# Kernel tuning notes

Hardware: AMD Instinct MI355X
Metric: run time of the kernel (lower is better)

## Reference

```python
import jax, jax.numpy as jnp
import numpy as np

B, H, W = 8, 56, 56
DIM_IN = 1792 + 2   # concatenated pyramid channels + 2 coord channels
D_OUT = 1792 // 4   # gamma_d = 4
N_CENTERS = H * W   # gamma_c = 1
K = 3


def avg_pool3(x):
    # F.avg_pool2d(x, 3, 1, 1) with count_include_pad=True: padded sum / 9
    s = jax.lax.reduce_window(x, 0.0, jax.lax.add, (1, 1, 3, 3), (1, 1, 1, 1),
                              ((0, 0), (0, 0), (1, 1), (1, 1)))
    return s / 9.0


def setup_inputs() -> dict:
    key = jax.random.key(0)
    k0, k1, k2, kw, kb, kc = jax.random.split(key, 6)
    p0 = jax.random.normal(k0, (B, 256, H, W), dtype=jnp.float32)
    p1 = jax.random.normal(k1, (B, 512, 28, 28), dtype=jnp.float32)
    p2 = jax.random.normal(k2, (B, 1024, 14, 14), dtype=jnp.float32)
    conv_w = jax.random.normal(kw, (D_OUT, DIM_IN), dtype=jnp.float32) * 0.02
    conv_b = jax.random.normal(kb, (D_OUT,), dtype=jnp.float32) * 0.01
    C = jax.random.normal(kc, (D_OUT, N_CENTERS), dtype=jnp.float32) * 0.5
    return {"p0": p0, "p1": p1, "p2": p2, "conv_w": conv_w, "conv_b": conv_b, "C": C}


def reference(p0, p1, p2, conv_w, conv_b, C):
    # Descriptor: avg-pool each level, upsample to first level, concat channels
    o0 = avg_pool3(p0)
    o1 = avg_pool3(p1)
    o2 = avg_pool3(p2)
    o1 = jax.image.resize(o1, (B, o1.shape[1], H, W), method='bilinear')  # align_corners=False equiv (upsample)
    o2 = jax.image.resize(o2, (B, o2.shape[1], H, W), method='bilinear')
    sample = jnp.concatenate([o0, o1, o2], axis=1)  # (B, 1792, H, W)

    # AddCoords: xx = row index / (H-1), yy = col index / (W-1), both *2-1
    xx = (jnp.arange(H, dtype=jnp.float32) / (H - 1) * 2 - 1)[:, None] * jnp.ones((1, W), jnp.float32)
    yy = (jnp.arange(W, dtype=jnp.float32) / (W - 1) * 2 - 1)[None, :] * jnp.ones((H, 1), jnp.float32)
    coords = jnp.broadcast_to(jnp.stack([xx, yy])[None], (B, 2, H, W))
    sample = jnp.concatenate([sample, coords], axis=1)  # (B, 1794, H, W)

    # 1x1 CoordConv
    phi = jnp.einsum('bchw,oc->bohw', sample, conv_w) + conv_b[None, :, None, None]
    phi_p = phi.transpose(0, 2, 3, 1).reshape(B, H * W, D_OUT)  # b (h w) c

    # squared distance to center bank via norm expansion
    feat2 = jnp.sum(phi_p ** 2, axis=2, keepdims=True)        # (B, HW, 1)
    cent2 = jnp.sum(C ** 2, axis=0)[None, None, :]            # (1, 1, N)
    dist = jnp.sqrt(feat2 + cent2 - 2.0 * jnp.matmul(phi_p, C))  # (B, HW, N)

    # top-K smallest, ascending
    neg_top, _ = jax.lax.top_k(-dist, K)
    topv = -neg_top                                           # (B, HW, K) ascending
    soft = jax.nn.softmax(-topv, axis=-1)                     # softmin
    score = soft[:, :, 0] * topv[:, :, 0]                     # (B, HW)
    return score.reshape(B, 1, H, W)
```

## Files before the change

### kernel.cpp

```cpp
#include <hip/hip_runtime.h>
#include <math.h>

#define B_    8
#define H_    56
#define W_    56
#define HW_   3136
#define C0_   256
#define C1_   512
#define C2_   1024
#define DIN_  1794
#define KD_   1792
#define KCP_  56
#define DOUT_ 448
#define NCHP_ 28
#define NC_   3136
#define NCHD_ 196
#define KCD_  14
#define DTS_  452
#define PCH_  28672

typedef __attribute__((ext_vector_type(8))) short bh8;
typedef __attribute__((ext_vector_type(4))) float f32x4;

__device__ __forceinline__ short f2bf(float f) {
  union { float f; unsigned u; } v; v.f = f;
  unsigned r = v.u + 0x7fffu + ((v.u >> 16) & 1u);
  return (short)(r >> 16);
}
__device__ __forceinline__ float bf2f(short s) {
  union { unsigned u; float f; } v; v.u = ((unsigned)(unsigned short)s) << 16;
  return v.f;
}

__global__ __launch_bounds__(256) void desc0_kernel(const float* __restrict__ p0,
                                                    short* __restrict__ desc) {
  __shared__ float sv[64 * 57];
  const int c0 = blockIdx.x * 64, h = blockIdx.y, b = blockIdx.z;
  for (int item = threadIdx.x; item < 64 * 56; item += 256) {
    int x = item % 56, c = item / 56;
    const float* src = p0 + (((size_t)(b * C0_ + c0 + c)) * 56 + h) * 56 + x;
    float s = src[0];
    if (h > 0)  s += src[-56];
    if (h < 55) s += src[56];
    sv[c * 57 + x] = s;
  }
  __syncthreads();
  for (int item = threadIdx.x; item < 56 * 8; item += 256) {
    int g = item & 7, w = item >> 3;
    bh8 o;
#pragma unroll
    for (int j = 0; j < 8; ++j) {
      const float* s0 = sv + (g * 8 + j) * 57;
      float v = s0[w];
      if (w > 0)  v += s0[w - 1];
      if (w < 55) v += s0[w + 1];
      o[j] = f2bf(v * (1.0f / 9.0f));
    }
    size_t pid = (size_t)b * HW_ + h * 56 + w;
    *(bh8*)(desc + pid * KD_ + c0 + g * 8) = o;
  }
}

__global__ __launch_bounds__(256) void desc1_kernel(const float* __restrict__ p1,
                                                    short* __restrict__ desc) {
  __shared__ float sv[2 * 64 * 29];
  const int c0 = blockIdx.x * 64, h = blockIdx.y, b = blockIdx.z;
  float sy = (h + 0.5f) * 0.5f - 0.5f;
  float fyf = floorf(sy);
  float fy = sy - fyf;
  int iy = (int)fyf;
  int pya = min(max(iy, 0), 27), pyb = min(max(iy + 1, 0), 27);
  for (int item = threadIdx.x; item < 64 * 2 * 28; item += 256) {
    int x = item % 28;
    int pr = (item / 28) & 1;
    int c = item / 56;
    int r = pr ? pyb : pya;
    const float* src = p1 + (((size_t)(b * C1_ + c0 + c)) * 28 + r) * 28 + x;
    float s = src[0];
    if (r > 0)  s += src[-28];
    if (r < 27) s += src[28];
    sv[pr * (64 * 29) + c * 29 + x] = s;
  }
  __syncthreads();
  for (int item = threadIdx.x; item < 56 * 8; item += 256) {
    int g = item & 7, w = item >> 3;
    float sx = (w + 0.5f) * 0.5f - 0.5f;
    float fxf = floorf(sx);
    float fx = sx - fxf;
    int ix = (int)fxf;
    int x0 = min(max(ix, 0), 27), x1 = min(max(ix + 1, 0), 27);
    bh8 o;
#pragma unroll
    for (int j = 0; j < 8; ++j) {
      const float* s0 = sv + (g * 8 + j) * 29;
      const float* s1 = s0 + 64 * 29;
      float p00 = s0[x0] + (x0 > 0 ? s0[x0 - 1] : 0.f) + (x0 < 27 ? s0[x0 + 1] : 0.f);
      float p01 = s0[x1] + (x1 > 0 ? s0[x1 - 1] : 0.f) + (x1 < 27 ? s0[x1 + 1] : 0.f);
      float p10 = s1[x0] + (x0 > 0 ? s1[x0 - 1] : 0.f) + (x0 < 27 ? s1[x0 + 1] : 0.f);
      float p11 = s1[x1] + (x1 > 0 ? s1[x1 - 1] : 0.f) + (x1 < 27 ? s1[x1 + 1] : 0.f);
      float top = p00 + fx * (p01 - p00);
      float bot = p10 + fx * (p11 - p10);
      o[j] = f2bf((top + fy * (bot - top)) * (1.0f / 9.0f));
    }
    size_t pid = (size_t)b * HW_ + h * 56 + w;
    *(bh8*)(desc + pid * KD_ + C0_ + c0 + g * 8) = o;
  }
}

__global__ __launch_bounds__(256) void desc2_kernel(const float* __restrict__ p2,
                                                    short* __restrict__ desc) {
  __shared__ float sv[2 * 64 * 15];
  const int c0 = blockIdx.x * 64, h = blockIdx.y, b = blockIdx.z;
  float sy = (h + 0.5f) * 0.25f - 0.5f;
  float fyf = floorf(sy);
  float fy = sy - fyf;
  int iy = (int)fyf;
  int pya = min(max(iy, 0), 13), pyb = min(max(iy + 1, 0), 13);
  for (int item = threadIdx.x; item < 64 * 2 * 14; item += 256) {
    int x = item % 14;
    int pr = (item / 14) & 1;
    int c = item / 28;
    int r = pr ? pyb : pya;
    const float* src = p2 + (((size_t)(b * C2_ + c0 + c)) * 14 + r) * 14 + x;
    float s = src[0];
    if (r > 0)  s += src[-14];
    if (r < 13) s += src[14];
    sv[pr * (64 * 15) + c * 15 + x] = s;
  }
  __syncthreads();
  for (int item = threadIdx.x; item < 56 * 8; item += 256) {
    int g = item & 7, w = item >> 3;
    float sx = (w + 0.5f) * 0.25f - 0.5f;
    float fxf = floorf(sx);
    float fx = sx - fxf;
    int ix = (int)fxf;
    int x0 = min(max(ix, 0), 13), x1 = min(max(ix + 1, 0), 13);
    bh8 o;
#pragma unroll
    for (int j = 0; j < 8; ++j) {
      const float* s0 = sv + (g * 8 + j) * 15;
      const float* s1 = s0 + 64 * 15;
      float p00 = s0[x0] + (x0 > 0 ? s0[x0 - 1] : 0.f) + (x0 < 13 ? s0[x0 + 1] : 0.f);
      float p01 = s0[x1] + (x1 > 0 ? s0[x1 - 1] : 0.f) + (x1 < 13 ? s0[x1 + 1] : 0.f);
      float p10 = s1[x0] + (x0 > 0 ? s1[x0 - 1] : 0.f) + (x0 < 13 ? s1[x0 + 1] : 0.f);
      float p11 = s1[x1] + (x1 > 0 ? s1[x1 - 1] : 0.f) + (x1 < 13 ? s1[x1 + 1] : 0.f);
      float top = p00 + fx * (p01 - p00);
      float bot = p10 + fx * (p11 - p10);
      o[j] = f2bf((top + fy * (bot - top)) * (1.0f / 9.0f));
    }
    size_t pid = (size_t)b * HW_ + h * 56 + w;
    *(bh8*)(desc + pid * KD_ + C0_ + C1_ + c0 + g * 8) = o;
  }
}

__global__ void cent2_kernel(const float* __restrict__ C, float* __restrict__ c2) {
  int j = blockIdx.x * blockDim.x + threadIdx.x;
  if (j >= NC_) return;
  float s = 0.f;
  for (int d = 0; d < DOUT_; ++d) {
    float v = bf2f(f2bf(C[(size_t)d * NC_ + j]));
    s = fmaf(v, v, s);
  }
  c2[j] = s;
}

__global__ void cpack_kernel(const float* __restrict__ C, short* __restrict__ Cpk) {
  int idx = blockIdx.x * 256 + threadIdx.x;
  int ln = idx & 63;
  int kc = (idx >> 6) % KCD_;
  int nc = idx / (KCD_ * 64);
  int n  = nc * 16 + (ln & 15);
  int k0 = kc * 32 + ((ln >> 4) << 3);
  bh8 o;
#pragma unroll
  for (int j = 0; j < 8; ++j) o[j] = f2bf(C[(size_t)(k0 + j) * NC_ + n]);
  *(bh8*)(Cpk + (size_t)idx * 8) = o;
}

__global__ void wpack_kernel(const float* __restrict__ W, short* __restrict__ Wpk) {
  int idx = blockIdx.x * 256 + threadIdx.x;
  int ln = idx & 63;
  int kc = (idx >> 6) % KCP_;
  int nc = idx / (KCP_ * 64);
  int n  = nc * 16 + (ln & 15);
  int k0 = kc * 32 + ((ln >> 4) << 3);
  bh8 o;
#pragma unroll
  for (int j = 0; j < 8; ++j) o[j] = f2bf(W[(size_t)n * DIN_ + k0 + j]);
  *(bh8*)(Wpk + (size_t)idx * 8) = o;
}

__global__ __launch_bounds__(256) void phi_mfma(
    const short* __restrict__ desc, const short* __restrict__ Wpk,
    const float* __restrict__ cw, const float* __restrict__ cb,
    short* __restrict__ phip ) {
  __shared__ __align__(16) float Dt[16 * DTS_];
  const int wv = threadIdx.x >> 6, ln = threadIdx.x & 63;
  const int pix0 = blockIdx.x * 32;
  const short* aptr = desc + ((size_t)(pix0 + (ln & 15))) * KD_ + ((ln >> 4) << 3);

  f32x4 acc[2][7];
#pragma unroll
  for (int rc = 0; rc < 2; ++rc)
#pragma unroll
    for (int i = 0; i < 7; ++i) acc[rc][i] = (f32x4){0.f, 0.f, 0.f, 0.f};

  const short* bbase = Wpk + (size_t)(wv * 7) * (KCP_ * 512) + ln * 8;
  for (int kc = 0; kc < KCP_; ++kc) {
    bh8 a0 = *(const bh8*)(aptr + kc * 32);
    bh8 a1 = *(const bh8*)(aptr + 16 * KD_ + kc * 32);
    const short* bp = bbase + kc * 512;
#pragma unroll
    for (int i = 0; i < 7; ++i) {
      bh8 bfr = *(const bh8*)(bp + (size_t)i * (KCP_ * 512));
      acc[0][i] = __builtin_amdgcn_mfma_f32_16x16x32_bf16(a0, bfr, acc[0][i], 0, 0, 0);
      acc[1][i] = __builtin_amdgcn_mfma_f32_16x16x32_bf16(a1, bfr, acc[1][i], 0, 0, 0);
    }
  }

  for (int rc = 0; rc < 2; ++rc) {
    __syncthreads();
#pragma unroll
    for (int i = 0; i < 7; ++i) {
      int col = (wv * 7 + i) * 16 + (ln & 15);
      float bias = cb[col];
      float wx = cw[(size_t)col * DIN_ + 1792];
      float wy = cw[(size_t)col * DIN_ + 1793];
#pragma unroll
      for (int r = 0; r < 4; ++r) {
        int row = ((ln >> 4) << 2) + r;
        int pid = pix0 + rc * 16 + row;
        int hw = pid % HW_;
        int hh = hw / 56, ww = hw % 56;
        float xx = (float)hh * (2.0f / 55.0f) - 1.0f;
        float yy = (float)ww * (2.0f / 55.0f) - 1.0f;
        Dt[row * DTS_ + col] = acc[rc][i][r] + bias + wx * xx + wy * yy;
      }
    }
    __syncthreads();
    short* op = phip + (size_t)(blockIdx.x * 2 + rc) * PCH_;
    for (int item = threadIdx.x; item < KCD_ * 64; item += 256) {
      int kc = item >> 6, lp = item & 63;
      int m = lp & 15, k0 = kc * 32 + ((lp >> 4) << 3);
      bh8 o;
#pragma unroll
      for (int j = 0; j < 8; ++j) o[j] = f2bf(Dt[m * DTS_ + k0 + j]);
      *(bh8*)(op + (size_t)item * 8) = o;
    }
  }
}

__device__ __forceinline__ void insert3(float& t0, float& t1, float& t2, float v) {
  if (v < t2) {
    if (v < t1) {
      t2 = t1;
      if (v < t0) { t1 = t0; t0 = v; } else t1 = v;
    } else t2 = v;
  }
}
__device__ __forceinline__ void merge3(float& a0, float& a1, float& a2,
                                       float b0, float b1, float b2) {
  float lo0 = fminf(a0, b0), hi0 = fmaxf(a0, b0);
  float lo1 = fminf(a1, b1), hi1 = fmaxf(a1, b1);
  float lo2 = fminf(a2, b2);
  a0 = lo0;
  a1 = fminf(hi0, lo1);
  a2 = fminf(fmaxf(hi0, lo1), fminf(hi1, lo2));
}
__device__ __forceinline__ float sumsq8(bh8 a, float s) {
#pragma unroll
  for (int j = 0; j < 8; ++j) { float v = bf2f(a[j]); s = fmaf(v, v, s); }
  return s;
}

#define KLIST(X) X(0) X(1) X(2) X(3) X(4) X(5) X(6) X(7) X(8) X(9) X(10) X(11) X(12) X(13)

__global__ __launch_bounds__(256, 4) void dist_part(
    const short* __restrict__ phip, const short* __restrict__ Cpk,
    const float* __restrict__ c2g, float* __restrict__ part) {
  __shared__ __align__(16) short Asl[14336];
  __shared__ float tri[4][16][4];
  const int wv = threadIdx.x >> 6, ln = threadIdx.x & 63;
  const int chunk = blockIdx.x;

  {
    const short* g_ = phip + (size_t)chunk * PCH_ + wv * 3584 + ln * 8;
    short* l_ = Asl + wv * 3584;
#pragma unroll
    for (int j = 0; j < 7; ++j)
      __builtin_amdgcn_global_load_lds(
          (const __attribute__((address_space(1))) unsigned int*)(g_ + j * 512),
          (__attribute__((address_space(3))) unsigned int*)(l_ + j * 512),
          16, 0, 0);
  }
  __syncthreads();

  const short* alds = Asl + ln * 8;

  float sum = 0.f;
#pragma unroll
  for (int i = 0; i < 14; ++i) sum = sumsq8(*(const bh8*)(alds + i * 512), sum);
  sum += __shfl_xor(sum, 16, 64);
  sum += __shfl_xor(sum, 32, 64);
  const int rb = (ln >> 4) << 2;
  float f2r0 = __shfl(sum, rb + 0, 64);
  float f2r1 = __shfl(sum, rb + 1, 64);
  float f2r2 = __shfl(sum, rb + 2, 64);
  float f2r3 = __shfl(sum, rb + 3, 64);

  float t00 = 1e30f, t01 = 1e30f, t02 = 1e30f;
  float t10 = 1e30f, t11 = 1e30f, t12 = 1e30f;
  float t20 = 1e30f, t21 = 1e30f, t22 = 1e30f;
  float t30 = 1e30f, t31 = 1e30f, t32 = 1e30f;

  const short* cb = Cpk + (size_t)wv * 49 * (KCD_ * 512) + ln * 8;
  const float* c2b = c2g + wv * 49 * 16 + (ln & 15);

  for (int nc = 0; nc < 49; ++nc) {
    const short* bp = cb + (size_t)nc * (KCD_ * 512);
#define LB(kc) bh8 B##kc = *(const bh8*)(bp + (kc) * 512);
    KLIST(LB)
#undef LB
    f32x4 acc = {0.f, 0.f, 0.f, 0.f};
#define MF(kc) acc = __builtin_amdgcn_mfma_f32_16x16x32_bf16( \
        *(const bh8*)(alds + (kc) * 512), B##kc, acc, 0, 0, 0);
    KLIST(MF)
#undef MF
    float c2v = c2b[nc * 16];
    insert3(t00, t01, t02, f2r0 + c2v - 2.0f * acc[0]);
    insert3(t10, t11, t12, f2r1 + c2v - 2.0f * acc[1]);
    insert3(t20, t21, t22, f2r2 + c2v - 2.0f * acc[2]);
    insert3(t30, t31, t32, f2r3 + c2v - 2.0f * acc[3]);
  }

#pragma unroll
  for (int m = 1; m <= 8; m <<= 1) {
    float b0, b1, b2;
    b0 = __shfl_xor(t00, m, 64); b1 = __shfl_xor(t01, m, 64); b2 = __shfl_xor(t02, m, 64);
    merge3(t00, t01, t02, b0, b1, b2);
    b0 = __shfl_xor(t10, m, 64); b1 = __shfl_xor(t11, m, 64); b2 = __shfl_xor(t12, m, 64);
    merge3(t10, t11, t12, b0, b1, b2);
    b0 = __shfl_xor(t20, m, 64); b1 = __shfl_xor(t21, m, 64); b2 = __shfl_xor(t22, m, 64);
    merge3(t20, t21, t22, b0, b1, b2);
    b0 = __shfl_xor(t30, m, 64); b1 = __shfl_xor(t31, m, 64); b2 = __shfl_xor(t32, m, 64);
    merge3(t30, t31, t32, b0, b1, b2);
  }

  if ((ln & 15) == 0) {
    tri[wv][rb + 0][0] = t00; tri[wv][rb + 0][1] = t01; tri[wv][rb + 0][2] = t02;
    tri[wv][rb + 1][0] = t10; tri[wv][rb + 1][1] = t11; tri[wv][rb + 1][2] = t12;
    tri[wv][rb + 2][0] = t20; tri[wv][rb + 2][1] = t21; tri[wv][rb + 2][2] = t22;
    tri[wv][rb + 3][0] = t30; tri[wv][rb + 3][1] = t31; tri[wv][rb + 3][2] = t32;
  }
  __syncthreads();
  if (threadIdx.x < 32) {
    int p = threadIdx.x & 15, hh = threadIdx.x >> 4;
    float a0 = tri[2 * hh][p][0], a1 = tri[2 * hh][p][1], a2 = tri[2 * hh][p][2];
    merge3(a0, a1, a2, tri[2 * hh + 1][p][0], tri[2 * hh + 1][p][1], tri[2 * hh + 1][p][2]);
    float* o = part + ((size_t)(chunk * 16 + p)) * 8 + hh * 4;
    o[0] = a0; o[1] = a1; o[2] = a2;
  }
}

__global__ __launch_bounds__(256) void merge_kernel(const float* __restrict__ part,
                                                    float* __restrict__ out) {
  int p = blockIdx.x * 256 + threadIdx.x;
  const float* q = part + (size_t)p * 8;
  float a0 = q[0], a1 = q[1], a2 = q[2];
  merge3(a0, a1, a2, q[4], q[5], q[6]);
  float d0 = sqrtf(fmaxf(a0, 0.f));
  float d1 = sqrtf(fmaxf(a1, 0.f));
  float d2 = sqrtf(fmaxf(a2, 0.f));
  float s0 = 1.0f / (1.0f + expf(d0 - d1) + expf(d0 - d2));
  out[p] = s0 * d0;
}

extern "C" void kernel_launch(void* const* d_in, const int* in_sizes, int n_in,
                              void* d_out, int out_size, void* d_ws, size_t ws_size,
                              hipStream_t stream) {
  const float* p0 = (const float*)d_in[0];
  const float* p1 = (const float*)d_in[1];
  const float* p2 = (const float*)d_in[2];
  const float* cw = (const float*)d_in[3];
  const float* cb = (const float*)d_in[4];
  const float* C  = (const float*)d_in[5];
  float* out = (float*)d_out;

  short* desc = (short*)d_ws;
  short* Cpk  = desc + (size_t)25088 * KD_;
  short* Wpk  = Cpk + (size_t)NCHD_ * KCD_ * 512;
  float* c2   = (float*)(Wpk + (size_t)NCHP_ * KCP_ * 512);
  float* part = c2 + NC_;

  desc0_kernel<<<dim3(4, 56, 8),  256, 0, stream>>>(p0, desc);
  desc1_kernel<<<dim3(8, 56, 8),  256, 0, stream>>>(p1, desc);
  desc2_kernel<<<dim3(16, 56, 8), 256, 0, stream>>>(p2, desc);
  cent2_kernel<<<(NC_ + 255) / 256, 256, 0, stream>>>(C, c2);
  cpack_kernel<<<NCHD_ * KCD_ * 64 / 256, 256, 0, stream>>>(C, Cpk);
  wpack_kernel<<<NCHP_ * KCP_ * 64 / 256, 256, 0, stream>>>(cw, Wpk);
  phi_mfma<<<25088 / 32, 256, 0, stream>>>(desc, Wpk, cw, cb, desc);
  dist_part<<<1568, 256, 0, stream>>>(desc, Cpk, c2, part);
  merge_kernel<<<25088 / 256, 256, 0, stream>>>(part, out);
}
```

Before: 687.0 us.

## Retile distance GEMM into 2D LDS-staged tiles with partial top-3 merge

```diff
diff --git a/kernel.cpp b/kernel.cpp
--- a/kernel.cpp
+++ b/kernel.cpp
@@ -250,6 +250,27 @@
   }
 }
 
+__device__ __forceinline__ float sumsq8(bh8 a, float s) {
+#pragma unroll
+  for (int j = 0; j < 8; ++j) { float v = bf2f(a[j]); s = fmaf(v, v, s); }
+  return s;
+}
+
+__global__ __launch_bounds__(256) void f2_kernel(const short* __restrict__ phip,
+                                                 float* __restrict__ f2g) {
+  int p = blockIdx.x * 256 + threadIdx.x;
+  const short* base = phip + (size_t)(p >> 4) * PCH_ + (p & 15) * 8;
+  float s0 = 0.f, s1 = 0.f, s2 = 0.f, s3 = 0.f;
+  for (int kc = 0; kc < KCD_; ++kc) {
+    const short* b = base + kc * 512;
+    s0 = sumsq8(*(const bh8*)(b), s0);
+    s1 = sumsq8(*(const bh8*)(b + 128), s1);
+    s2 = sumsq8(*(const bh8*)(b + 256), s2);
+    s3 = sumsq8(*(const bh8*)(b + 384), s3);
+  }
+  f2g[p] = (s0 + s1) + (s2 + s3);
+}
+
 __device__ __forceinline__ void insert3(float& t0, float& t1, float& t2, float v) {
   if (v < t2) {
     if (v < t1) {
@@ -267,107 +288,125 @@
   a1 = fminf(hi0, lo1);
   a2 = fminf(fmaxf(hi0, lo1), fminf(hi1, lo2));
 }
-__device__ __forceinline__ float sumsq8(bh8 a, float s) {
-#pragma unroll
-  for (int j = 0; j < 8; ++j) { float v = bf2f(a[j]); s = fmaf(v, v, s); }
-  return s;
-}
-
-#define KLIST(X) X(0) X(1) X(2) X(3) X(4) X(5) X(6) X(7) X(8) X(9) X(10) X(11) X(12) X(13)
-
-__global__ __launch_bounds__(256, 4) void dist_part(
+
+__global__ __launch_bounds__(256) void dist_gemm(
     const short* __restrict__ phip, const short* __restrict__ Cpk,
-    const float* __restrict__ c2g, float* __restrict__ part) {
-  __shared__ __align__(16) short Asl[14336];
-  __shared__ float tri[4][16][4];
+    const float* __restrict__ c2g, const float* __restrict__ f2g,
+    short* __restrict__ p28s ) {
+  __shared__ __align__(16) short Asl[2][8192];
+  __shared__ __align__(16) short Bsl[2][7168];
   const int wv = threadIdx.x >> 6, ln = threadIdx.x & 63;
-  const int chunk = blockIdx.x;
-
-  {
-    const short* g_ = phip + (size_t)chunk * PCH_ + wv * 3584 + ln * 8;
-    short* l_ = Asl + wv * 3584;
-#pragma unroll
-    for (int j = 0; j < 7; ++j)
-      __builtin_amdgcn_global_load_lds(
-          (const __attribute__((address_space(1))) unsigned int*)(g_ + j * 512),
-          (__attribute__((address_space(3))) unsigned int*)(l_ + j * 512),
-          16, 0, 0);
-  }
+  const int mt = blockIdx.x / 28, nt = blockIdx.x % 28;
+  const int c0 = mt * 8;
+  const int n0 = nt * 7;
+
+#define STG(buf, t) { \
+    _Pragma("unroll") \
+    for (int q_ = 0; q_ < 4; ++q_) { \
+      int f_ = wv * 4 + q_; \
+      const short* g_ = phip + (size_t)(c0 + (f_ >> 1)) * PCH_ + (2 * (t) + (f_ & 1)) * 512 + ln * 8; \
+      __builtin_amdgcn_global_load_lds( \
+          (const __attribute__((address_space(1))) unsigned int*)g_, \
+          (__attribute__((address_space(3))) unsigned int*)(&Asl[(buf)][f_ * 512]), 16, 0, 0); \
+    } \
+    _Pragma("unroll") \
+    for (int q_ = 0; q_ < 4; ++q_) { \
+      int f_ = wv * 4 + q_; \
+      if (f_ < 14) { \
+        const short* g_ = Cpk + (size_t)(n0 + (f_ >> 1)) * (KCD_ * 512) + (2 * (t) + (f_ & 1)) * 512 + ln * 8; \
+        __builtin_amdgcn_global_load_lds( \
+            (const __attribute__((address_space(1))) unsigned int*)g_, \
+            (__attribute__((address_space(3))) unsigned int*)(&Bsl[(buf)][f_ * 512]), 16, 0, 0); \
+      } \
+    } }
+
+  f32x4 acc[2][7];
+#pragma unroll
+  for (int mi = 0; mi < 2; ++mi)
+#pragma unroll
+    for (int nc = 0; nc < 7; ++nc) acc[mi][nc] = (f32x4){0.f, 0.f, 0.f, 0.f};
+
+  STG(0, 0)
   __syncthreads();
 
-  const short* alds = Asl + ln * 8;
-
-  float sum = 0.f;
-#pragma unroll
-  for (int i = 0; i < 14; ++i) sum = sumsq8(*(const bh8*)(alds + i * 512), sum);
-  sum += __shfl_xor(sum, 16, 64);
-  sum += __shfl_xor(sum, 32, 64);
-  const int rb = (ln >> 4) << 2;
-  float f2r0 = __shfl(sum, rb + 0, 64);
-  float f2r1 = __shfl(sum, rb + 1, 64);
-  float f2r2 = __shfl(sum, rb + 2, 64);
-  float f2r3 = __shfl(sum, rb + 3, 64);
-
-  float t00 = 1e30f, t01 = 1e30f, t02 = 1e30f;
-  float t10 = 1e30f, t11 = 1e30f, t12 = 1e30f;
-  float t20 = 1e30f, t21 = 1e30f, t22 = 1e30f;
-  float t30 = 1e30f, t31 = 1e30f, t32 = 1e30f;
-
-  const short* cb = Cpk + (size_t)wv * 49 * (KCD_ * 512) + ln * 8;
-  const float* c2b = c2g + wv * 49 * 16 + (ln & 15);
-
-  for (int nc = 0; nc < 49; ++nc) {
-    const short* bp = cb + (size_t)nc * (KCD_ * 512);
-#define LB(kc) bh8 B##kc = *(const bh8*)(bp + (kc) * 512);
-    KLIST(LB)
-#undef LB
-    f32x4 acc = {0.f, 0.f, 0.f, 0.f};
-#define MF(kc) acc = __builtin_amdgcn_mfma_f32_16x16x32_bf16( \
-        *(const bh8*)(alds + (kc) * 512), B##kc, acc, 0, 0, 0);
-    KLIST(MF)
-#undef MF
-    float c2v = c2b[nc * 16];
-    insert3(t00, t01, t02, f2r0 + c2v - 2.0f * acc[0]);
-    insert3(t10, t11, t12, f2r1 + c2v - 2.0f * acc[1]);
-    insert3(t20, t21, t22, f2r2 + c2v - 2.0f * acc[2]);
-    insert3(t30, t31, t32, f2r3 + c2v - 2.0f * acc[3]);
-  }
+  for (int t = 0; t < 7; ++t) {
+    if (t < 6) STG((t + 1) & 1, t + 1)
+    const short* ab = &Asl[t & 1][0] + ln * 8;
+    const short* bb = &Bsl[t & 1][0] + ln * 8;
+#pragma unroll
+    for (int j = 0; j < 2; ++j) {
+      bh8 a0 = *(const bh8*)(ab + ((2 * wv + 0) * 2 + j) * 512);
+      bh8 a1 = *(const bh8*)(ab + ((2 * wv + 1) * 2 + j) * 512);
+#pragma unroll
+      for (int nc = 0; nc < 7; ++nc) {
+        bh8 bf = *(const bh8*)(bb + (nc * 2 + j) * 512);
+        acc[0][nc] = __builtin_amdgcn_mfma_f32_16x16x32_bf16(a0, bf, acc[0][nc], 0, 0, 0);
+        acc[1][nc] = __builtin_amdgcn_mfma_f32_16x16x32_bf16(a1, bf, acc[1][nc], 0, 0, 0);
+      }
+    }
+    __syncthreads();
+  }
+#undef STG
+
+  const int col = ln & 15, rb = (ln >> 4) << 2;
+  float c2v[7];
+#pragma unroll
+  for (int nc = 0; nc < 7; ++nc) c2v[nc] = c2g[(n0 + nc) * 16 + col];
+  float f2p[2][4];
+#pragma unroll
+  for (int mi = 0; mi < 2; ++mi)
+#pragma unroll
+    for (int r = 0; r < 4; ++r)
+      f2p[mi][r] = f2g[(size_t)(c0 + 2 * wv + mi) * 16 + rb + r];
+
+  float t0[2][4], t1[2][4], t2[2][4];
+#pragma unroll
+  for (int mi = 0; mi < 2; ++mi)
+#pragma unroll
+    for (int r = 0; r < 4; ++r) { t0[mi][r] = 1e30f; t1[mi][r] = 1e30f; t2[mi][r] = 1e30f; }
+
+#pragma unroll
+  for (int nc = 0; nc < 7; ++nc)
+#pragma unroll
+    for (int mi = 0; mi < 2; ++mi)
+#pragma unroll
+      for (int r = 0; r < 4; ++r)
+        insert3(t0[mi][r], t1[mi][r], t2[mi][r],
+                f2p[mi][r] + c2v[nc] - 2.0f * acc[mi][nc][r]);
 
 #pragma unroll
   for (int m = 1; m <= 8; m <<= 1) {
-    float b0, b1, b2;
-    b0 = __shfl_xor(t00, m, 64); b1 = __shfl_xor(t01, m, 64); b2 = __shfl_xor(t02, m, 64);
-    merge3(t00, t01, t02, b0, b1, b2);
-    b0 = __shfl_xor(t10, m, 64); b1 = __shfl_xor(t11, m, 64); b2 = __shfl_xor(t12, m, 64);
-    merge3(t10, t11, t12, b0, b1, b2);
-    b0 = __shfl_xor(t20, m, 64); b1 = __shfl_xor(t21, m, 64); b2 = __shfl_xor(t22, m, 64);
-    merge3(t20, t21, t22, b0, b1, b2);
-    b0 = __shfl_xor(t30, m, 64); b1 = __shfl_xor(t31, m, 64); b2 = __shfl_xor(t32, m, 64);
-    merge3(t30, t31, t32, b0, b1, b2);
-  }
-
-  if ((ln & 15) == 0) {
-    tri[wv][rb + 0][0] = t00; tri[wv][rb + 0][1] = t01; tri[wv][rb + 0][2] = t02;
-    tri[wv][rb + 1][0] = t10; tri[wv][rb + 1][1] = t11; tri[wv][rb + 1][2] = t12;
-    tri[wv][rb + 2][0] = t20; tri[wv][rb + 2][1] = t21; tri[wv][rb + 2][2] = t22;
-    tri[wv][rb + 3][0] = t30; tri[wv][rb + 3][1] = t31; tri[wv][rb + 3][2] = t32;
-  }
-  __syncthreads();
-  if (threadIdx.x < 32) {
-    int p = threadIdx.x & 15, hh = threadIdx.x >> 4;
-    float a0 = tri[2 * hh][p][0], a1 = tri[2 * hh][p][1], a2 = tri[2 * hh][p][2];
-    merge3(a0, a1, a2, tri[2 * hh + 1][p][0], tri[2 * hh + 1][p][1], tri[2 * hh + 1][p][2]);
-    float* o = part + ((size_t)(chunk * 16 + p)) * 8 + hh * 4;
-    o[0] = a0; o[1] = a1; o[2] = a2;
-  }
-}
-
-__global__ __launch_bounds__(256) void merge_kernel(const float* __restrict__ part,
-                                                    float* __restrict__ out) {
+#pragma unroll
+    for (int mi = 0; mi < 2; ++mi)
+#pragma unroll
+      for (int r = 0; r < 4; ++r) {
+        float b0 = __shfl_xor(t0[mi][r], m, 64);
+        float b1 = __shfl_xor(t1[mi][r], m, 64);
+        float b2 = __shfl_xor(t2[mi][r], m, 64);
+        merge3(t0[mi][r], t1[mi][r], t2[mi][r], b0, b1, b2);
+      }
+  }
+
+  if (col == 0) {
+#pragma unroll
+    for (int mi = 0; mi < 2; ++mi) {
+      float* o = (float*)(p28s + (size_t)(c0 + 2 * wv + mi) * PCH_ + 7168);
+#pragma unroll
+      for (int r = 0; r < 4; ++r) {
+        float* q = o + ((size_t)(rb + r) * 28 + nt) * 4;
+        q[0] = t0[mi][r]; q[1] = t1[mi][r]; q[2] = t2[mi][r];
+      }
+    }
+  }
+}
+
+__global__ __launch_bounds__(256) void merge28_kernel(const short* __restrict__ p28s,
+                                                      float* __restrict__ out) {
   int p = blockIdx.x * 256 + threadIdx.x;
-  const float* q = part + (size_t)p * 8;
+  const float* q = (const float*)(p28s + (size_t)(p >> 4) * PCH_ + 7168) + (p & 15) * 112;
   float a0 = q[0], a1 = q[1], a2 = q[2];
-  merge3(a0, a1, a2, q[4], q[5], q[6]);
+  for (int nt = 1; nt < 28; ++nt)
+    merge3(a0, a1, a2, q[nt * 4], q[nt * 4 + 1], q[nt * 4 + 2]);
   float d0 = sqrtf(fmaxf(a0, 0.f));
   float d1 = sqrtf(fmaxf(a1, 0.f));
   float d2 = sqrtf(fmaxf(a2, 0.f));
@@ -390,7 +429,7 @@
   short* Cpk  = desc + (size_t)25088 * KD_;
   short* Wpk  = Cpk + (size_t)NCHD_ * KCD_ * 512;
   float* c2   = (float*)(Wpk + (size_t)NCHP_ * KCP_ * 512);
-  float* part = c2 + NC_;
+  float* f2g  = c2 + NC_;
 
   desc0_kernel<<<dim3(4, 56, 8),  256, 0, stream>>>(p0, desc);
   desc1_kernel<<<dim3(8, 56, 8),  256, 0, stream>>>(p1, desc);
@@ -399,6 +438,7 @@
   cpack_kernel<<<NCHD_ * KCD_ * 64 / 256, 256, 0, stream>>>(C, Cpk);
   wpack_kernel<<<NCHP_ * KCP_ * 64 / 256, 256, 0, stream>>>(cw, Wpk);
   phi_mfma<<<25088 / 32, 256, 0, stream>>>(desc, Wpk, cw, cb, desc);
-  dist_part<<<1568, 256, 0, stream>>>(desc, Cpk, c2, part);
-  merge_kernel<<<25088 / 256, 256, 0, stream>>>(part, out);
-}
+  f2_kernel<<<25088 / 256, 256, 0, stream>>>(desc, f2g);
+  dist_gemm<<<196 * 28, 256, 0, stream>>>(desc, Cpk, c2, f2g, desc);
+  merge28_kernel<<<25088 / 256, 256, 0, stream>>>(desc, out);
+}
```

After: 718.0 us. 1.05x slower.

## Restructure distance kernel to tile centers in LDS and stream phi chunks

Applied to the files above, without the earlier changes.

```diff
diff --git a/kernel.cpp b/kernel.cpp
--- a/kernel.cpp
+++ b/kernel.cpp
@@ -250,6 +250,11 @@
   }
 }
 
+__device__ __forceinline__ float sumsq8(bh8 a, float s) {
+#pragma unroll
+  for (int j = 0; j < 8; ++j) { float v = bf2f(a[j]); s = fmaf(v, v, s); }
+  return s;
+}
 __device__ __forceinline__ void insert3(float& t0, float& t1, float& t2, float v) {
   if (v < t2) {
     if (v < t1) {
@@ -267,107 +272,139 @@
   a1 = fminf(hi0, lo1);
   a2 = fminf(fmaxf(hi0, lo1), fminf(hi1, lo2));
 }
-__device__ __forceinline__ float sumsq8(bh8 a, float s) {
-#pragma unroll
-  for (int j = 0; j < 8; ++j) { float v = bf2f(a[j]); s = fmaf(v, v, s); }
-  return s;
-}
-
-#define KLIST(X) X(0) X(1) X(2) X(3) X(4) X(5) X(6) X(7) X(8) X(9) X(10) X(11) X(12) X(13)
-
-__global__ __launch_bounds__(256, 4) void dist_part(
+
+__global__ __launch_bounds__(256) void f2_kernel(const short* __restrict__ phip,
+                                                 float* __restrict__ f2g) {
+  int p = blockIdx.x * 256 + threadIdx.x;
+  const short* base = phip + (size_t)(p >> 4) * PCH_ + (p & 15) * 8;
+  float s0 = 0.f, s1 = 0.f, s2 = 0.f, s3 = 0.f;
+  for (int kc = 0; kc < KCD_; ++kc) {
+    const short* b = base + kc * 512;
+    s0 = sumsq8(*(const bh8*)(b), s0);
+    s1 = sumsq8(*(const bh8*)(b + 128), s1);
+    s2 = sumsq8(*(const bh8*)(b + 256), s2);
+    s3 = sumsq8(*(const bh8*)(b + 384), s3);
+  }
+  f2g[p] = (s0 + s1) + (s2 + s3);
+}
+
+
+#define LOADSET(S, ch) { \
+    const short* ap_ = phip + (size_t)(ch) * PCH_ + ln * 8; \
+    S##0  = *(const bh8*)(ap_ +  0 * 512); S##1  = *(const bh8*)(ap_ +  1 * 512); \
+    S##2  = *(const bh8*)(ap_ +  2 * 512); S##3  = *(const bh8*)(ap_ +  3 * 512); \
+    S##4  = *(const bh8*)(ap_ +  4 * 512); S##5  = *(const bh8*)(ap_ +  5 * 512); \
+    S##6  = *(const bh8*)(ap_ +  6 * 512); S##7  = *(const bh8*)(ap_ +  7 * 512); \
+    S##8  = *(const bh8*)(ap_ +  8 * 512); S##9  = *(const bh8*)(ap_ +  9 * 512); \
+    S##10 = *(const bh8*)(ap_ + 10 * 512); S##11 = *(const bh8*)(ap_ + 11 * 512); \
+    S##12 = *(const bh8*)(ap_ + 12 * 512); S##13 = *(const bh8*)(ap_ + 13 * 512); }
+
+#define MK(S, kc) \
+    a0 = __builtin_amdgcn_mfma_f32_16x16x32_bf16(S##kc, *(const bh8*)(bl + (0 * 14 + (kc)) * 512), a0, 0, 0, 0); \
+    a1 = __builtin_amdgcn_mfma_f32_16x16x32_bf16(S##kc, *(const bh8*)(bl + (1 * 14 + (kc)) * 512), a1, 0, 0, 0); \
+    a2 = __builtin_amdgcn_mfma_f32_16x16x32_bf16(S##kc, *(const bh8*)(bl + (2 * 14 + (kc)) * 512), a2, 0, 0, 0); \
+    a3 = __builtin_amdgcn_mfma_f32_16x16x32_bf16(S##kc, *(const bh8*)(bl + (3 * 14 + (kc)) * 512), a3, 0, 0, 0);
+
+#define COMPUTE(S, ch) { \
+    f32x4 a0 = {0.f, 0.f, 0.f, 0.f}, a1 = a0, a2 = a0, a3 = a0; \
+    MK(S, 0) MK(S, 1) MK(S, 2) MK(S, 3) MK(S, 4) MK(S, 5) MK(S, 6) \
+    MK(S, 7) MK(S, 8) MK(S, 9) MK(S, 10) MK(S, 11) MK(S, 12) MK(S, 13) \
+    float fr0 = f2g[(size_t)(ch) * 16 + rb + 0]; \
+    float fr1 = f2g[(size_t)(ch) * 16 + rb + 1]; \
+    float fr2 = f2g[(size_t)(ch) * 16 + rb + 2]; \
+    float fr3 = f2g[(size_t)(ch) * 16 + rb + 3]; \
+    float c20 = c2g[(nt4 + 0) * 16 + col], c21 = c2g[(nt4 + 1) * 16 + col]; \
+    float c22 = c2g[(nt4 + 2) * 16 + col], c23 = c2g[(nt4 + 3) * 16 + col]; \
+    float t00 = 1e30f, t01 = 1e30f, t02 = 1e30f; \
+    float t10 = 1e30f, t11 = 1e30f, t12 = 1e30f; \
+    float t20 = 1e30f, t21 = 1e30f, t22 = 1e30f; \
+    float t30 = 1e30f, t31 = 1e30f, t32 = 1e30f; \
+    insert3(t00, t01, t02, fr0 + c20 - 2.0f * a0[0]); \
+    insert3(t10, t11, t12, fr1 + c20 - 2.0f * a0[1]); \
+    insert3(t20, t21, t22, fr2 + c20 - 2.0f * a0[2]); \
+    insert3(t30, t31, t32, fr3 + c20 - 2.0f * a0[3]); \
+    insert3(t00, t01, t02, fr0 + c21 - 2.0f * a1[0]); \
+    insert3(t10, t11, t12, fr1 + c21 - 2.0f * a1[1]); \
+    insert3(t20, t21, t22, fr2 + c21 - 2.0f * a1[2]); \
+    insert3(t30, t31, t32, fr3 + c21 - 2.0f * a1[3]); \
+    insert3(t00, t01, t02, fr0 + c22 - 2.0f * a2[0]); \
+    insert3(t10, t11, t12, fr1 + c22 - 2.0f * a2[1]); \
+    insert3(t20, t21, t22, fr2 + c22 - 2.0f * a2[2]); \
+    insert3(t30, t31, t32, fr3 + c22 - 2.0f * a2[3]); \
+    insert3(t00, t01, t02, fr0 + c23 - 2.0f * a3[0]); \
+    insert3(t10, t11, t12, fr1 + c23 - 2.0f * a3[1]); \
+    insert3(t20, t21, t22, fr2 + c23 - 2.0f * a3[2]); \
+    insert3(t30, t31, t32, fr3 + c23 - 2.0f * a3[3]); \
+    _Pragma("unroll") \
+    for (int m_ = 1; m_ <= 8; m_ <<= 1) { \
+      float b0, b1, b2; \
+      b0 = __shfl_xor(t00, m_, 64); b1 = __shfl_xor(t01, m_, 64); b2 = __shfl_xor(t02, m_, 64); \
+      merge3(t00, t01, t02, b0, b1, b2); \
+      b0 = __shfl_xor(t10, m_, 64); b1 = __shfl_xor(t11, m_, 64); b2 = __shfl_xor(t12, m_, 64); \
+      merge3(t10, t11, t12, b0, b1, b2); \
+      b0 = __shfl_xor(t20, m_, 64); b1 = __shfl_xor(t21, m_, 64); b2 = __shfl_xor(t22, m_, 64); \
+      merge3(t20, t21, t22, b0, b1, b2); \
+      b0 = __shfl_xor(t30, m_, 64); b1 = __shfl_xor(t31, m_, 64); b2 = __shfl_xor(t32, m_, 64); \
+      merge3(t30, t31, t32, b0, b1, b2); \
+    } \
+    if (col == 0) { \
+      float* o_ = (float*)(p49s + (size_t)(ch) * PCH_ + 7168); \
+      float* q_; \
+      q_ = o_ + ((size_t)(rb + 0) * 49 + nt) * 4; q_[0] = t00; q_[1] = t01; q_[2] = t02; \
+      q_ = o_ + ((size_t)(rb + 1) * 49 + nt) * 4; q_[0] = t10; q_[1] = t11; q_[2] = t12; \
+      q_ = o_ + ((size_t)(rb + 2) * 49 + nt) * 4; q_[0] = t20; q_[1] = t21; q_[2] = t22; \
+      q_ = o_ + ((size_t)(rb + 3) * 49 + nt) * 4; q_[0] = t30; q_[1] = t31; q_[2] = t32; \
+    } }
+
+__global__ __launch_bounds__(256, 2) void dist_nt(
     const short* __restrict__ phip, const short* __restrict__ Cpk,
-    const float* __restrict__ c2g, float* __restrict__ part) {
-  __shared__ __align__(16) short Asl[14336];
-  __shared__ float tri[4][16][4];
+    const float* __restrict__ c2g, const float* __restrict__ f2g,
+    short* __restrict__ p49s ) {
+  __shared__ __align__(16) short Bsl[56 * 512];
   const int wv = threadIdx.x >> 6, ln = threadIdx.x & 63;
-  const int chunk = blockIdx.x;
+  const int nt = blockIdx.x % 49;
+  const int mg = blockIdx.x / 49;
+  const int nt4 = nt * 4;
+  const int col = ln & 15, rb = (ln >> 4) << 2;
 
   {
-    const short* g_ = phip + (size_t)chunk * PCH_ + wv * 3584 + ln * 8;
-    short* l_ = Asl + wv * 3584;
-#pragma unroll
-    for (int j = 0; j < 7; ++j)
+    const short* g_ = Cpk + (size_t)(nt4 + wv) * (KCD_ * 512) + ln * 8;
+#pragma unroll
+    for (int q = 0; q < 14; ++q)
       __builtin_amdgcn_global_load_lds(
-          (const __attribute__((address_space(1))) unsigned int*)(g_ + j * 512),
-          (__attribute__((address_space(3))) unsigned int*)(l_ + j * 512),
+          (const __attribute__((address_space(1))) unsigned int*)(g_ + q * 512),
+          (__attribute__((address_space(3))) unsigned int*)(&Bsl[(wv * 14 + q) * 512]),
           16, 0, 0);
   }
+
+  const short* bl = (const short*)Bsl + ln * 8;
+  const int cw = mg * 16 + wv * 4;
+
+  bh8 XA0, XA1, XA2, XA3, XA4, XA5, XA6, XA7, XA8, XA9, XA10, XA11, XA12, XA13;
+  bh8 YA0, YA1, YA2, YA3, YA4, YA5, YA6, YA7, YA8, YA9, YA10, YA11, YA12, YA13;
+
+  LOADSET(XA, cw)
+  LOADSET(YA, cw + 1)
   __syncthreads();
 
-  const short* alds = Asl + ln * 8;
-
-  float sum = 0.f;
-#pragma unroll
-  for (int i = 0; i < 14; ++i) sum = sumsq8(*(const bh8*)(alds + i * 512), sum);
-  sum += __shfl_xor(sum, 16, 64);
-  sum += __shfl_xor(sum, 32, 64);
-  const int rb = (ln >> 4) << 2;
-  float f2r0 = __shfl(sum, rb + 0, 64);
-  float f2r1 = __shfl(sum, rb + 1, 64);
-  float f2r2 = __shfl(sum, rb + 2, 64);
-  float f2r3 = __shfl(sum, rb + 3, 64);
-
-  float t00 = 1e30f, t01 = 1e30f, t02 = 1e30f;
-  float t10 = 1e30f, t11 = 1e30f, t12 = 1e30f;
-  float t20 = 1e30f, t21 = 1e30f, t22 = 1e30f;
-  float t30 = 1e30f, t31 = 1e30f, t32 = 1e30f;
-
-  const short* cb = Cpk + (size_t)wv * 49 * (KCD_ * 512) + ln * 8;
-  const float* c2b = c2g + wv * 49 * 16 + (ln & 15);
-
-  for (int nc = 0; nc < 49; ++nc) {
-    const short* bp = cb + (size_t)nc * (KCD_ * 512);
-#define LB(kc) bh8 B##kc = *(const bh8*)(bp + (kc) * 512);
-    KLIST(LB)
-#undef LB
-    f32x4 acc = {0.f, 0.f, 0.f, 0.f};
-#define MF(kc) acc = __builtin_amdgcn_mfma_f32_16x16x32_bf16( \
-        *(const bh8*)(alds + (kc) * 512), B##kc, acc, 0, 0, 0);
-    KLIST(MF)
-#undef MF
-    float c2v = c2b[nc * 16];
-    insert3(t00, t01, t02, f2r0 + c2v - 2.0f * acc[0]);
-    insert3(t10, t11, t12, f2r1 + c2v - 2.0f * acc[1]);
-    insert3(t20, t21, t22, f2r2 + c2v - 2.0f * acc[2]);
-    insert3(t30, t31, t32, f2r3 + c2v - 2.0f * acc[3]);
-  }
-
-#pragma unroll
-  for (int m = 1; m <= 8; m <<= 1) {
-    float b0, b1, b2;
-    b0 = __shfl_xor(t00, m, 64); b1 = __shfl_xor(t01, m, 64); b2 = __shfl_xor(t02, m, 64);
-    merge3(t00, t01, t02, b0, b1, b2);
-    b0 = __shfl_xor(t10, m, 64); b1 = __shfl_xor(t11, m, 64); b2 = __shfl_xor(t12, m, 64);
-    merge3(t10, t11, t12, b0, b1, b2);
-    b0 = __shfl_xor(t20, m, 64); b1 = __shfl_xor(t21, m, 64); b2 = __shfl_xor(t22, m, 64);
-    merge3(t20, t21, t22, b0, b1, b2);
-    b0 = __shfl_xor(t30, m, 64); b1 = __shfl_xor(t31, m, 64); b2 = __shfl_xor(t32, m, 64);
-    merge3(t30, t31, t32, b0, b1, b2);
-  }
-
-  if ((ln & 15) == 0) {
-    tri[wv][rb + 0][0] = t00; tri[wv][rb + 0][1] = t01; tri[wv][rb + 0][2] = t02;
-    tri[wv][rb + 1][0] = t10; tri[wv][rb + 1][1] = t11; tri[wv][rb + 1][2] = t12;
-    tri[wv][rb + 2][0] = t20; tri[wv][rb + 2][1] = t21; tri[wv][rb + 2][2] = t22;
-    tri[wv][rb + 3][0] = t30; tri[wv][rb + 3][1] = t31; tri[wv][rb + 3][2] = t32;
-  }
-  __syncthreads();
-  if (threadIdx.x < 32) {
-    int p = threadIdx.x & 15, hh = threadIdx.x >> 4;
-    float a0 = tri[2 * hh][p][0], a1 = tri[2 * hh][p][1], a2 = tri[2 * hh][p][2];
-    merge3(a0, a1, a2, tri[2 * hh + 1][p][0], tri[2 * hh + 1][p][1], tri[2 * hh + 1][p][2]);
-    float* o = part + ((size_t)(chunk * 16 + p)) * 8 + hh * 4;
-    o[0] = a0; o[1] = a1; o[2] = a2;
-  }
-}
-
-__global__ __launch_bounds__(256) void merge_kernel(const float* __restrict__ part,
-                                                    float* __restrict__ out) {
+  COMPUTE(XA, cw)
+  LOADSET(XA, cw + 2)
+  __builtin_amdgcn_sched_barrier(0);
+  COMPUTE(YA, cw + 1)
+  LOADSET(YA, cw + 3)
+  __builtin_amdgcn_sched_barrier(0);
+  COMPUTE(XA, cw + 2)
+  COMPUTE(YA, cw + 3)
+}
+
+__global__ __launch_bounds__(256) void merge49_kernel(const short* __restrict__ p49s,
+                                                      float* __restrict__ out) {
   int p = blockIdx.x * 256 + threadIdx.x;
-  const float* q = part + (size_t)p * 8;
+  const float* q = (const float*)(p49s + (size_t)(p >> 4) * PCH_ + 7168)
+                   + (size_t)(p & 15) * 196;
   float a0 = q[0], a1 = q[1], a2 = q[2];
-  merge3(a0, a1, a2, q[4], q[5], q[6]);
+  for (int nt = 1; nt < 49; ++nt)
+    merge3(a0, a1, a2, q[nt * 4], q[nt * 4 + 1], q[nt * 4 + 2]);
   float d0 = sqrtf(fmaxf(a0, 0.f));
   float d1 = sqrtf(fmaxf(a1, 0.f));
   float d2 = sqrtf(fmaxf(a2, 0.f));
@@ -390,7 +427,7 @@
   short* Cpk  = desc + (size_t)25088 * KD_;
   short* Wpk  = Cpk + (size_t)NCHD_ * KCD_ * 512;
   float* c2   = (float*)(Wpk + (size_t)NCHP_ * KCP_ * 512);
-  float* part = c2 + NC_;
+  float* f2g  = c2 + NC_;
 
   desc0_kernel<<<dim3(4, 56, 8),  256, 0, stream>>>(p0, desc);
   desc1_kernel<<<dim3(8, 56, 8),  256, 0, stream>>>(p1, desc);
@@ -399,6 +436,7 @@
   cpack_kernel<<<NCHD_ * KCD_ * 64 / 256, 256, 0, stream>>>(C, Cpk);
   wpack_kernel<<<NCHP_ * KCP_ * 64 / 256, 256, 0, stream>>>(cw, Wpk);
   phi_mfma<<<25088 / 32, 256, 0, stream>>>(desc, Wpk, cw, cb, desc);
-  dist_part<<<1568, 256, 0, stream>>>(desc, Cpk, c2, part);
-  merge_kernel<<<25088 / 256, 256, 0, stream>>>(part, out);
-}
+  f2_kernel<<<25088 / 256, 256, 0, stream>>>(desc, f2g);
+  dist_nt<<<49 * 98, 256, 0, stream>>>(desc, Cpk, c2, f2g, desc);
+  merge49_kernel<<<25088 / 256, 256, 0, stream>>>(desc, out);
+}
```

Result: no change. 681.9 us (-0.7%).

## Retile distance GEMM with center tiles in LDS and XCD-aware block swizzle

Applied to the files above, without the earlier changes.

```diff
diff --git a/kernel.cpp b/kernel.cpp
--- a/kernel.cpp
+++ b/kernel.cpp
@@ -250,6 +250,11 @@
   }
 }
 
+__device__ __forceinline__ float sumsq8(bh8 a, float s) {
+#pragma unroll
+  for (int j = 0; j < 8; ++j) { float v = bf2f(a[j]); s = fmaf(v, v, s); }
+  return s;
+}
 __device__ __forceinline__ void insert3(float& t0, float& t1, float& t2, float v) {
   if (v < t2) {
     if (v < t1) {
@@ -267,107 +272,131 @@
   a1 = fminf(hi0, lo1);
   a2 = fminf(fmaxf(hi0, lo1), fminf(hi1, lo2));
 }
-__device__ __forceinline__ float sumsq8(bh8 a, float s) {
-#pragma unroll
-  for (int j = 0; j < 8; ++j) { float v = bf2f(a[j]); s = fmaf(v, v, s); }
-  return s;
-}
-
-#define KLIST(X) X(0) X(1) X(2) X(3) X(4) X(5) X(6) X(7) X(8) X(9) X(10) X(11) X(12) X(13)
-
-__global__ __launch_bounds__(256, 4) void dist_part(
+
+__global__ __launch_bounds__(256) void f2_kernel(const short* __restrict__ phip,
+                                                 float* __restrict__ f2g) {
+  int p = blockIdx.x * 256 + threadIdx.x;
+  const short* base = phip + (size_t)(p >> 4) * PCH_ + (p & 15) * 8;
+  float s0 = 0.f, s1 = 0.f, s2 = 0.f, s3 = 0.f;
+  for (int kc = 0; kc < KCD_; ++kc) {
+    const short* b = base + kc * 512;
+    s0 = sumsq8(*(const bh8*)(b), s0);
+    s1 = sumsq8(*(const bh8*)(b + 128), s1);
+    s2 = sumsq8(*(const bh8*)(b + 256), s2);
+    s3 = sumsq8(*(const bh8*)(b + 384), s3);
+  }
+  f2g[p] = (s0 + s1) + (s2 + s3);
+}
+
+__global__ __launch_bounds__(256, 2) void dist_nt(
     const short* __restrict__ phip, const short* __restrict__ Cpk,
-    const float* __restrict__ c2g, float* __restrict__ part) {
-  __shared__ __align__(16) short Asl[14336];
-  __shared__ float tri[4][16][4];
+    const float* __restrict__ c2g, const float* __restrict__ f2g,
+    short* __restrict__ p49s ) {
+  __shared__ __align__(16) short Bsl[56 * 512];
   const int wv = threadIdx.x >> 6, ln = threadIdx.x & 63;
-  const int chunk = blockIdx.x;
+  const int orig = blockIdx.x;
+  const int xcd = orig & 7, bi = orig >> 3;
+  const int swz = (xcd < 2) ? xcd * 601 + bi : 1202 + (xcd - 2) * 600 + bi;
+  const int nt = swz % 49;
+  const int mg = swz / 49;
+  const int nt4 = nt * 4;
+  const int col = ln & 15, rb = (ln >> 4) << 2;
 
   {
-    const short* g_ = phip + (size_t)chunk * PCH_ + wv * 3584 + ln * 8;
-    short* l_ = Asl + wv * 3584;
-#pragma unroll
-    for (int j = 0; j < 7; ++j)
+    const short* g_ = Cpk + (size_t)(nt4 + wv) * (KCD_ * 512) + ln * 8;
+#pragma unroll
+    for (int q = 0; q < 14; ++q)
       __builtin_amdgcn_global_load_lds(
-          (const __attribute__((address_space(1))) unsigned int*)(g_ + j * 512),
-          (__attribute__((address_space(3))) unsigned int*)(l_ + j * 512),
+          (const __attribute__((address_space(1))) unsigned int*)(g_ + q * 512),
+          (__attribute__((address_space(3))) unsigned int*)(&Bsl[(wv * 14 + q) * 512]),
           16, 0, 0);
   }
   __syncthreads();
 
-  const short* alds = Asl + ln * 8;
-
-  float sum = 0.f;
-#pragma unroll
-  for (int i = 0; i < 14; ++i) sum = sumsq8(*(const bh8*)(alds + i * 512), sum);
-  sum += __shfl_xor(sum, 16, 64);
-  sum += __shfl_xor(sum, 32, 64);
-  const int rb = (ln >> 4) << 2;
-  float f2r0 = __shfl(sum, rb + 0, 64);
-  float f2r1 = __shfl(sum, rb + 1, 64);
-  float f2r2 = __shfl(sum, rb + 2, 64);
-  float f2r3 = __shfl(sum, rb + 3, 64);
-
-  float t00 = 1e30f, t01 = 1e30f, t02 = 1e30f;
-  float t10 = 1e30f, t11 = 1e30f, t12 = 1e30f;
-  float t20 = 1e30f, t21 = 1e30f, t22 = 1e30f;
-  float t30 = 1e30f, t31 = 1e30f, t32 = 1e30f;
-
-  const short* cb = Cpk + (size_t)wv * 49 * (KCD_ * 512) + ln * 8;
-  const float* c2b = c2g + wv * 49 * 16 + (ln & 15);
-
-  for (int nc = 0; nc < 49; ++nc) {
-    const short* bp = cb + (size_t)nc * (KCD_ * 512);
-#define LB(kc) bh8 B##kc = *(const bh8*)(bp + (kc) * 512);
-    KLIST(LB)
-#undef LB
-    f32x4 acc = {0.f, 0.f, 0.f, 0.f};
-#define MF(kc) acc = __builtin_amdgcn_mfma_f32_16x16x32_bf16( \
-        *(const bh8*)(alds + (kc) * 512), B##kc, acc, 0, 0, 0);
-    KLIST(MF)
-#undef MF
-    float c2v = c2b[nc * 16];
-    insert3(t00, t01, t02, f2r0 + c2v - 2.0f * acc[0]);
-    insert3(t10, t11, t12, f2r1 + c2v - 2.0f * acc[1]);
-    insert3(t20, t21, t22, f2r2 + c2v - 2.0f * acc[2]);
-    insert3(t30, t31, t32, f2r3 + c2v - 2.0f * acc[3]);
-  }
-
-#pragma unroll
-  for (int m = 1; m <= 8; m <<= 1) {
-    float b0, b1, b2;
-    b0 = __shfl_xor(t00, m, 64); b1 = __shfl_xor(t01, m, 64); b2 = __shfl_xor(t02, m, 64);
-    merge3(t00, t01, t02, b0, b1, b2);
-    b0 = __shfl_xor(t10, m, 64); b1 = __shfl_xor(t11, m, 64); b2 = __shfl_xor(t12, m, 64);
-    merge3(t10, t11, t12, b0, b1, b2);
-    b0 = __shfl_xor(t20, m, 64); b1 = __shfl_xor(t21, m, 64); b2 = __shfl_xor(t22, m, 64);
-    merge3(t20, t21, t22, b0, b1, b2);
-    b0 = __shfl_xor(t30, m, 64); b1 = __shfl_xor(t31, m, 64); b2 = __shfl_xor(t32, m, 64);
-    merge3(t30, t31, t32, b0, b1, b2);
-  }
-
-  if ((ln & 15) == 0) {
-    tri[wv][rb + 0][0] = t00; tri[wv][rb + 0][1] = t01; tri[wv][rb + 0][2] = t02;
-    tri[wv][rb + 1][0] = t10; tri[wv][rb + 1][1] = t11; tri[wv][rb + 1][2] = t12;
-    tri[wv][rb + 2][0] = t20; tri[wv][rb + 2][1] = t21; tri[wv][rb + 2][2] = t22;
-    tri[wv][rb + 3][0] = t30; tri[wv][rb + 3][1] = t31; tri[wv][rb + 3][2] = t32;
-  }
-  __syncthreads();
-  if (threadIdx.x < 32) {
-    int p = threadIdx.x & 15, hh = threadIdx.x >> 4;
-    float a0 = tri[2 * hh][p][0], a1 = tri[2 * hh][p][1], a2 = tri[2 * hh][p][2];
-    merge3(a0, a1, a2, tri[2 * hh + 1][p][0], tri[2 * hh + 1][p][1], tri[2 * hh + 1][p][2]);
-    float* o = part + ((size_t)(chunk * 16 + p)) * 8 + hh * 4;
-    o[0] = a0; o[1] = a1; o[2] = a2;
-  }
-}
-
-__global__ __launch_bounds__(256) void merge_kernel(const float* __restrict__ part,
-                                                    float* __restrict__ out) {
+  const short* bl = (const short*)Bsl + ln * 8;
+  const float c20 = c2g[(nt4 + 0) * 16 + col];
+  const float c21 = c2g[(nt4 + 1) * 16 + col];
+  const float c22 = c2g[(nt4 + 2) * 16 + col];
+  const float c23 = c2g[(nt4 + 3) * 16 + col];
+  const int cw = mg * 16 + wv * 4;
+
+#pragma unroll 1
+  for (int cc = 0; cc < 4; ++cc) {
+    const int ch = cw + cc;
+    const short* ap_ = phip + (size_t)ch * PCH_ + ln * 8;
+    bh8 A0  = *(const bh8*)(ap_ +  0 * 512), A1  = *(const bh8*)(ap_ +  1 * 512);
+    bh8 A2  = *(const bh8*)(ap_ +  2 * 512), A3  = *(const bh8*)(ap_ +  3 * 512);
+    bh8 A4  = *(const bh8*)(ap_ +  4 * 512), A5  = *(const bh8*)(ap_ +  5 * 512);
+    bh8 A6  = *(const bh8*)(ap_ +  6 * 512), A7  = *(const bh8*)(ap_ +  7 * 512);
+    bh8 A8  = *(const bh8*)(ap_ +  8 * 512), A9  = *(const bh8*)(ap_ +  9 * 512);
+    bh8 A10 = *(const bh8*)(ap_ + 10 * 512), A11 = *(const bh8*)(ap_ + 11 * 512);
+    bh8 A12 = *(const bh8*)(ap_ + 12 * 512), A13 = *(const bh8*)(ap_ + 13 * 512);
+    f32x4 a0 = {0.f, 0.f, 0.f, 0.f}, a1 = a0, a2 = a0, a3 = a0;
+#define MK(kc) \
+    a0 = __builtin_amdgcn_mfma_f32_16x16x32_bf16(A##kc, *(const bh8*)(bl + (0 * 14 + (kc)) * 512), a0, 0, 0, 0); \
+    a1 = __builtin_amdgcn_mfma_f32_16x16x32_bf16(A##kc, *(const bh8*)(bl + (1 * 14 + (kc)) * 512), a1, 0, 0, 0); \
+    a2 = __builtin_amdgcn_mfma_f32_16x16x32_bf16(A##kc, *(const bh8*)(bl + (2 * 14 + (kc)) * 512), a2, 0, 0, 0); \
+    a3 = __builtin_amdgcn_mfma_f32_16x16x32_bf16(A##kc, *(const bh8*)(bl + (3 * 14 + (kc)) * 512), a3, 0, 0, 0);
+    MK(0) MK(1) MK(2) MK(3) MK(4) MK(5) MK(6)
+    MK(7) MK(8) MK(9) MK(10) MK(11) MK(12) MK(13)
+#undef MK
+    float fr0 = f2g[(size_t)ch * 16 + rb + 0];
+    float fr1 = f2g[(size_t)ch * 16 + rb + 1];
+    float fr2 = f2g[(size_t)ch * 16 + rb + 2];
+    float fr3 = f2g[(size_t)ch * 16 + rb + 3];
+    float t00 = 1e30f, t01 = 1e30f, t02 = 1e30f;
+    float t10 = 1e30f, t11 = 1e30f, t12 = 1e30f;
+    float t20 = 1e30f, t21 = 1e30f, t22 = 1e30f;
+    float t30 = 1e30f, t31 = 1e30f, t32 = 1e30f;
+    insert3(t00, t01, t02, fr0 + c20 - 2.0f * a0[0]);
+    insert3(t10, t11, t12, fr1 + c20 - 2.0f * a0[1]);
+    insert3(t20, t21, t22, fr2 + c20 - 2.0f * a0[2]);
+    insert3(t30, t31, t32, fr3 + c20 - 2.0f * a0[3]);
+    insert3(t00, t01, t02, fr0 + c21 - 2.0f * a1[0]);
+    insert3(t10, t11, t12, fr1 + c21 - 2.0f * a1[1]);
+    insert3(t20, t21, t22, fr2 + c21 - 2.0f * a1[2]);
+    insert3(t30, t31, t32, fr3 + c21 - 2.0f * a1[3]);
+    insert3(t00, t01, t02, fr0 + c22 - 2.0f * a2[0]);
+    insert3(t10, t11, t12, fr1 + c22 - 2.0f * a2[1]);
+    insert3(t20, t21, t22, fr2 + c22 - 2.0f * a2[2]);
+    insert3(t30, t31, t32, fr3 + c22 - 2.0f * a2[3]);
+    insert3(t00, t01, t02, fr0 + c23 - 2.0f * a3[0]);
+    insert3(t10, t11, t12, fr1 + c23 - 2.0f * a3[1]);
+    insert3(t20, t21, t22, fr2 + c23 - 2.0f * a3[2]);
+    insert3(t30, t31, t32, fr3 + c23 - 2.0f * a3[3]);
+#pragma unroll
+    for (int m_ = 1; m_ <= 8; m_ <<= 1) {
+      float b0, b1, b2;
+      b0 = __shfl_xor(t00, m_, 64); b1 = __shfl_xor(t01, m_, 64); b2 = __shfl_xor(t02, m_, 64);
+      merge3(t00, t01, t02, b0, b1, b2);
+      b0 = __shfl_xor(t10, m_, 64); b1 = __shfl_xor(t11, m_, 64); b2 = __shfl_xor(t12, m_, 64);
+      merge3(t10, t11, t12, b0, b1, b2);
+      b0 = __shfl_xor(t20, m_, 64); b1 = __shfl_xor(t21, m_, 64); b2 = __shfl_xor(t22, m_, 64);
+      merge3(t20, t21, t22, b0, b1, b2);
+      b0 = __shfl_xor(t30, m_, 64); b1 = __shfl_xor(t31, m_, 64); b2 = __shfl_xor(t32, m_, 64);
+      merge3(t30, t31, t32, b0, b1, b2);
+    }
+    if (col == 0) {
+      float* o_ = (float*)(p49s + (size_t)ch * PCH_ + 7168);
+      float* q_;
+      q_ = o_ + ((size_t)nt * 16 + rb + 0) * 4; q_[0] = t00; q_[1] = t01; q_[2] = t02;
+      q_ = o_ + ((size_t)nt * 16 + rb + 1) * 4; q_[0] = t10; q_[1] = t11; q_[2] = t12;
+      q_ = o_ + ((size_t)nt * 16 + rb + 2) * 4; q_[0] = t20; q_[1] = t21; q_[2] = t22;
+      q_ = o_ + ((size_t)nt * 16 + rb + 3) * 4; q_[0] = t30; q_[1] = t31; q_[2] = t32;
+    }
+  }
+}
+
+__global__ __launch_bounds__(256) void merge49_kernel(const short* __restrict__ p49s,
+                                                      float* __restrict__ out) {
   int p = blockIdx.x * 256 + threadIdx.x;
-  const float* q = part + (size_t)p * 8;
-  float a0 = q[0], a1 = q[1], a2 = q[2];
-  merge3(a0, a1, a2, q[4], q[5], q[6]);
+  const float* base = (const float*)(p49s + (size_t)(p >> 4) * PCH_ + 7168);
+  const int row = p & 15;
+  float a0 = base[row * 4], a1 = base[row * 4 + 1], a2 = base[row * 4 + 2];
+  for (int nt = 1; nt < 49; ++nt) {
+    const float* q = base + ((size_t)nt * 16 + row) * 4;
+    merge3(a0, a1, a2, q[0], q[1], q[2]);
+  }
   float d0 = sqrtf(fmaxf(a0, 0.f));
   float d1 = sqrtf(fmaxf(a1, 0.f));
   float d2 = sqrtf(fmaxf(a2, 0.f));
@@ -390,7 +419,7 @@
   short* Cpk  = desc + (size_t)25088 * KD_;
   short* Wpk  = Cpk + (size_t)NCHD_ * KCD_ * 512;
   float* c2   = (float*)(Wpk + (size_t)NCHP_ * KCP_ * 512);
-  float* part = c2 + NC_;
+  float* f2g  = c2 + NC_;
 
   desc0_kernel<<<dim3(4, 56, 8),  256, 0, stream>>>(p0, desc);
   desc1_kernel<<<dim3(8, 56, 8),  256, 0, stream>>>(p1, desc);
@@ -399,6 +428,7 @@
   cpack_kernel<<<NCHD_ * KCD_ * 64 / 256, 256, 0, stream>>>(C, Cpk);
   wpack_kernel<<<NCHP_ * KCP_ * 64 / 256, 256, 0, stream>>>(cw, Wpk);
   phi_mfma<<<25088 / 32, 256, 0, stream>>>(desc, Wpk, cw, cb, desc);
-  dist_part<<<1568, 256, 0, stream>>>(desc, Cpk, c2, part);
-  merge_kernel<<<25088 / 256, 256, 0, stream>>>(part, out);
-}
+  f2_kernel<<<25088 / 256, 256, 0, stream>>>(desc, f2g);
+  dist_nt<<<49 * 98, 256, 0, stream>>>(desc, Cpk, c2, f2g, desc);
+  merge49_kernel<<<25088 / 256, 256, 0, stream>>>(desc, out);
+}
```

Result: faster. 661.1 us (-3.8%).
